# Optimization experiments

Measured on AMD Instinct MI355X. Metric: run time of the kernel, lower is better.

Reference implementation:

```python
import jax, jax.numpy as jnp
import numpy as np

MAX_ROUNDS = 6
MIN_ROUNDS = 2
WINDOW = 4
LAMBDA_P = 0.2
LN_EPS = 1e-5


def _mlp(x, W1, b1, W2, b2):
    # Linear -> exact GELU -> Linear (matches nn.Sequential(Linear, GELU, Linear))
    return jax.nn.gelu(x @ W1 + b1, approximate=False) @ W2 + b2


def _layernorm(x, g, b):
    m = x.mean(-1, keepdims=True)
    v = x.var(-1, keepdims=True)
    return (x - m) / jnp.sqrt(v + LN_EPS) * g + b


def setup_inputs() -> dict:
    key = jax.random.key(0)
    ks = jax.random.split(key, 13)
    B, N, D = 4, 2048, 512
    s = 0.02
    f32 = jnp.float32
    return {
        "summaries": jax.random.normal(ks[0], (B, N, D), f32),
        "msg_W1": jax.random.normal(ks[1], (2 * D, D), f32) * s,
        "msg_b1": jnp.zeros((D,), f32),
        "msg_W2": jax.random.normal(ks[2], (D, D), f32) * s,
        "msg_b2": jnp.zeros((D,), f32),
        "upd_W1": jax.random.normal(ks[3], (2 * D, D), f32) * s,
        "upd_b1": jnp.zeros((D,), f32),
        "upd_W2": jax.random.normal(ks[4], (D, D), f32) * s,
        "upd_b2": jnp.zeros((D,), f32),
        "halt_W": jax.random.normal(ks[5], (D, 1), f32) * s,
        "halt_b": jnp.zeros((1,), f32),
        "ln_g": jnp.ones((D,), f32),
        "ln_b": jnp.zeros((D,), f32),
    }


def reference(summaries, msg_W1, msg_b1, msg_W2, msg_b2,
              upd_W1, upd_b1, upd_W2, upd_b2,
              halt_W, halt_b, ln_g, ln_b):
    B, N, D = summaries.shape
    dt = summaries.dtype
    h = summaries
    remaining = jnp.ones((B, N, 1), dt)
    output = jnp.zeros_like(h)
    kl = jnp.zeros((), dt)
    done = jnp.asarray(False)  # emulates the early `break` under jit
    pos = jnp.arange(N)
    # number of valid causal neighbors of position i: min(i+1, window+1)
    counts = jnp.minimum(pos + 1, WINDOW + 1).astype(dt)[None, :, None]

    for step in range(MAX_ROUNDS):
        # windowed gather + message MLP, vectorized over the (W+1) offsets
        acc = jnp.zeros_like(h)
        for d in range(WINDOW + 1):
            nb = h if d == 0 else jnp.pad(h, ((0, 0), (d, 0), (0, 0)))[:, :N]
            m = _mlp(jnp.concatenate([h, nb], axis=-1), msg_W1, msg_b1, msg_W2, msg_b2)
            mask = (pos >= d).astype(dt)[None, :, None]
            acc = acc + m * mask
        msgs = acc / counts  # mean over valid neighbors, shape (B, N, D)

        new_h = h + _mlp(jnp.concatenate([h, msgs], axis=-1), upd_W1, upd_b1, upd_W2, upd_b2)
        h_next = _layernorm(new_h, ln_g, ln_b)

        if step < MIN_ROUNDS:
            halt = jnp.zeros((B, N, 1), dt)
        elif step == MAX_ROUNDS - 1:
            halt = jnp.ones((B, N, 1), dt)
        else:
            hp = jax.nn.sigmoid(h_next.mean(axis=1, keepdims=True) @ halt_W + halt_b)  # (B,1,1)
            halt = jnp.broadcast_to(hp, (B, N, 1))

        step_weight = remaining * halt
        out_next = output + step_weight * h_next
        rem_next = remaining * (1.0 - halt)

        p_geom = LAMBDA_P * (1.0 - LAMBDA_P) ** step
        # F.kl_div(log(q), log(p), log_target=True) = p * (log p - log q)
        kl_term = p_geom * (jnp.log(p_geom) - jnp.log(halt.mean() + 1e-8))

        active = jnp.logical_not(done)
        af = active.astype(dt)
        h = jnp.where(active, h_next, h)
        output = jnp.where(active, out_next, output)
        remaining = jnp.where(active, rem_next, remaining)
        kl = kl + af * kl_term.astype(dt)
        done = jnp.logical_or(done, remaining.max() < 0.01)

    return output, kl / MAX_ROUNDS
```

## Files before the change

kernel.cpp:

```cpp
#include <hip/hip_runtime.h>
#include <cmath>

#define DEV __device__ __forceinline__

typedef __bf16 bf16x8 __attribute__((ext_vector_type(8)));
typedef float f32x4v __attribute__((ext_vector_type(4)));
typedef unsigned short u16x8 __attribute__((ext_vector_type(8)));
typedef unsigned short u16x4 __attribute__((ext_vector_type(4)));

DEV float bf2f(unsigned short u){ return __uint_as_float(((unsigned)u)<<16); }
DEV unsigned short f2bf(float f){
  unsigned u = __float_as_uint(f);
  u = (u + 0x7fffu + ((u>>16)&1u)) >> 16;
  return (unsigned short)u;
}
DEV float geluf(float x){ return 0.5f*x*(1.0f + erff(x*0.7071067811865475f)); }

#define GLDS16(g,l) __builtin_amdgcn_global_load_lds(\
    (const __attribute__((address_space(1))) void*)(g), \
    (__attribute__((address_space(3))) void*)(l), 16, 0, 0)

#define NB    4
#define NSEQ  2048
#define DDIM  512
#define MROWS 8192

#define OFF_H     0u
#define OFF_HB    16777216u
#define OFF_UV    25165824u
#define OFF_GP    25165824u
#define OFF_R     33554432u
#define OFF_GSC   41943040u
#define OFF_WUV   50331648u
#define OFF_WP    51380224u
#define OFF_WR    52428800u
#define OFF_BUV   52953088u
#define OFF_BP    52957184u
#define OFF_BR    52959232u
#define OFF_DOT   52961280u
#define OFF_SCAL  52994048u
#define OFF_FLAGS 52994112u
#define OFF_A2    25165824u
#define OFF_B2    25690112u

__global__ __launch_bounds__(256) void k_prep_tr(
    const float* __restrict__ mW1, const float* __restrict__ uW2,
    const float* __restrict__ uW1,
    unsigned short* __restrict__ Wuv, unsigned short* __restrict__ Wr,
    unsigned short* __restrict__ Wp,  unsigned short* __restrict__ A2)
{
  __shared__ float t[64][65];
  const int tid = threadIdx.x, c = tid&63, r4 = tid>>6;
  const float* src; unsigned short* dst; int dld;
  switch (blockIdx.y){
    case 0: src = mW1;          dst = Wuv;          dld = 512;  break;
    case 1: src = mW1 + 262144; dst = Wuv + 262144; dld = 512;  break;
    case 2: src = uW2;          dst = Wr;           dld = 512;  break;
    case 3: src = uW1;          dst = Wp;           dld = 1024; break;
    default:src = uW1 + 262144; dst = A2;           dld = 512;  break;
  }
  const int k0 = (blockIdx.x>>3)<<6, n0 = (blockIdx.x&7)<<6;
  #pragma unroll
  for (int i=0;i<16;++i){ int r = i*4 + r4; t[r][c] = src[(size_t)(k0+r)*512 + n0 + c]; }
  __syncthreads();
  #pragma unroll
  for (int i=0;i<16;++i){ int r = i*4 + r4; dst[(size_t)(n0+r)*dld + k0 + c] = f2bf(t[c][r]); }
}

__global__ __launch_bounds__(256) void k_prep_small(
    const float* __restrict__ mW2, const float* __restrict__ mb1,
    const float* __restrict__ ub2,
    unsigned short* __restrict__ B2, float* __restrict__ biasUV,
    float* __restrict__ biasR)
{
  int idx = blockIdx.x*256 + threadIdx.x;
  if (idx < 262144)      B2[idx] = f2bf(mW2[idx]);
  else if (idx < 263168){ int j = idx-262144; biasUV[j] = (j<512)? mb1[j] : 0.f; }
  else if (idx < 263680){ int j = idx-263168; biasR[j] = ub2[j]; }
}

__global__ __launch_bounds__(256) void k_prep_biasP(
    const float* __restrict__ ub1, const float* __restrict__ mb2,
    const float* __restrict__ uW1, float* __restrict__ biasP)
{
  int n = blockIdx.x*256 + threadIdx.x;
  float s = ub1[n];
  for (int j=0;j<512;++j) s += mb2[j]*uW1[(512+j)*512+n];
  biasP[n] = s;
}

__global__ void k_init_state(float* scal, int* flags){
  int t = threadIdx.x;
  if (t<4) scal[t]=1.f;
  else if (t<9) scal[t]=0.f;
  if (t==9){ flags[0]=1; flags[1]=0; }
}

__global__ __launch_bounds__(256) void k_init_h(
    const float* __restrict__ S, float* __restrict__ H, u16x4* __restrict__ Hb)
{
  size_t idx = (size_t)blockIdx.x*256 + threadIdx.x;
  float4 v = ((const float4*)S)[idx];
  ((float4*)H)[idx] = v;
  u16x4 o; o[0]=f2bf(v.x); o[1]=f2bf(v.y); o[2]=f2bf(v.z); o[3]=f2bf(v.w);
  Hb[idx] = o;
}

template<int EPI>
__global__ __launch_bounds__(256) void k_gemm(
    const unsigned short* __restrict__ A0, const unsigned short* __restrict__ A1,
    const unsigned short* __restrict__ Bt, const float* __restrict__ bias,
    void* __restrict__ Cout, int ldc, int ldb, int nK, int ksplit, int gridN,
    const int* __restrict__ flags)
{
  if (flags[0]==0) return;
  __shared__ unsigned short sm[2][12288];
  const int tid = threadIdx.x;
  const int bid = blockIdx.x;
  const int nb  = (int)gridDim.x;
  const int ppx = (nb>>3)/gridN;
  int mp, np;
  if (ppx*gridN*8 == nb){ const int xcd = bid&7, ib = bid>>3; mp = xcd*ppx + ib/gridN; np = ib%gridN; }
  else                  { mp = bid/gridN; np = bid%gridN; }
  const int m0 = mp<<7, n0 = np<<6;
  const int sr = tid>>3;
  const int scA = (((tid&7) ^ (sr&7)) << 3);
  const int lane = tid&63, wv = tid>>6, wr = wv>>1, wc = wv&1;
  const int la = lane&15, lg = lane>>4;
  const int swzr = (la&7)<<3;
  f32x4v acc[4][2] = {};

  auto stage = [&](int ks, int bufi){
    const unsigned short* As = (ks<ksplit)? A0 : A1;
    const int kc = ((ks<ksplit)? ks : (ks-ksplit))<<6;
    unsigned short* s = sm[bufi];
    #pragma unroll
    for (int i=0;i<4;++i)
      GLDS16(As + (size_t)(m0 + i*32 + sr)*512 + kc + scA, s + i*2048 + tid*8);
    #pragma unroll
    for (int i=0;i<2;++i)
      GLDS16(Bt + (size_t)(n0 + i*32 + sr)*ldb + (ks<<6) + scA, s + 8192 + i*2048 + tid*8);
  };

  stage(0, 0);
  if (nK > 1) stage(1, 1);
  for (int ks=0; ks<nK; ++ks){
    const int cur = ks & 1;
    if (ks+1 < nK) asm volatile("s_waitcnt vmcnt(6)" ::: "memory");
    else           asm volatile("s_waitcnt vmcnt(0)" ::: "memory");
    __builtin_amdgcn_s_barrier();
    asm volatile("" ::: "memory");
    const unsigned short* s = sm[cur];
    #pragma unroll
    for (int kk=0;kk<2;++kk){
      bf16x8 af[4], bfr[2];
      #pragma unroll
      for (int mi=0;mi<4;++mi)
        af[mi] = *(const bf16x8*)(s + ((wr<<6) + (mi<<4) + la)*64 + (((kk<<5) + (lg<<3)) ^ swzr));
      #pragma unroll
      for (int ni=0;ni<2;++ni)
        bfr[ni] = *(const bf16x8*)(s + 8192 + ((wc<<5) + (ni<<4) + la)*64 + (((kk<<5) + (lg<<3)) ^ swzr));
      #pragma unroll
      for (int mi=0;mi<4;++mi)
        #pragma unroll
        for (int ni=0;ni<2;++ni)
          acc[mi][ni] = __builtin_amdgcn_mfma_f32_16x16x32_bf16(af[mi], bfr[ni], acc[mi][ni], 0, 0, 0);
    }
    asm volatile("" ::: "memory");
    __builtin_amdgcn_s_barrier();
    asm volatile("" ::: "memory");
    if (ks+2 < nK) stage(ks+2, cur);
  }

  const int r0 = m0 + (wr<<6) + (lg<<2);
  const int c0 = n0 + (wc<<5) + la;
  #pragma unroll
  for (int mi=0;mi<4;++mi){
    #pragma unroll
    for (int ni=0;ni<2;++ni){
      const int col = c0 + (ni<<4);
      const float bs = bias[col];
      #pragma unroll
      for (int r=0;r<4;++r){
        const int row = r0 + (mi<<4) + r;
        float v = acc[mi][ni][r] + bs;
        if constexpr (EPI==1) v = geluf(v);
        if constexpr (EPI==2) ((float*)Cout)[(size_t)row*ldc + col] = v;
        else ((unsigned short*)Cout)[(size_t)row*ldc + col] = f2bf(v);
      }
    }
  }
}

__global__ __launch_bounds__(256) void k_geluacc(
    const unsigned short* __restrict__ UV, unsigned short* __restrict__ G,
    const int* __restrict__ flags)
{
  if (flags[0]==0) return;
  int r = blockIdx.x*4 + (threadIdx.x>>6);
  int lane = threadIdx.x & 63;
  int c8 = lane*8;
  int i = r & (NSEQ-1);
  int nd = (i<4) ? i : 4;
  const u16x8 u = *(const u16x8*)(UV + (size_t)r*1024 + c8);
  float acc[8] = {0,0,0,0,0,0,0,0};
  for (int d=0; d<=nd; ++d){
    const u16x8 v = *(const u16x8*)(UV + (size_t)(r-d)*1024 + 512 + c8);
    #pragma unroll
    for (int j=0;j<8;++j) acc[j] += geluf(bf2f(u[j]) + bf2f(v[j]));
  }
  float inv = 1.0f/(float)(nd+1);
  u16x8 o;
  #pragma unroll
  for (int j=0;j<8;++j) o[j] = f2bf(acc[j]*inv);
  *(u16x8*)(G + (size_t)r*512 + c8) = o;
}

__global__ __launch_bounds__(256) void k_ln(
    const float* __restrict__ Rr, float* __restrict__ H, unsigned short* __restrict__ Hb,
    const float* __restrict__ gamma, const float* __restrict__ beta,
    const float* __restrict__ hW, float* __restrict__ DOT, float* __restrict__ OUT,
    const float* __restrict__ scal, const int* __restrict__ flags,
    int accmode, int dodot)
{
  const int lane = threadIdx.x & 63;
  const int row = (blockIdx.x<<2) + (threadIdx.x>>6);
  const int bidx = row >> 11;
  const size_t base = (size_t)row*512 + lane*8;
  float4 x0 = *(const float4*)(H+base);
  float4 x1 = *(const float4*)(H+base+4);

  if (accmode){
    const float w = scal[4+bidx];
    float4 o0, o1;
    if (accmode==1){
      o0 = make_float4(w*x0.x, w*x0.y, w*x0.z, w*x0.w);
      o1 = make_float4(w*x1.x, w*x1.y, w*x1.z, w*x1.w);
    } else {
      o0 = *(const float4*)(OUT+base);
      o1 = *(const float4*)(OUT+base+4);
      o0.x += w*x0.x; o0.y += w*x0.y; o0.z += w*x0.z; o0.w += w*x0.w;
      o1.x += w*x1.x; o1.y += w*x1.y; o1.z += w*x1.z; o1.w += w*x1.w;
    }
    *(float4*)(OUT+base)   = o0;
    *(float4*)(OUT+base+4) = o1;
  }
  if (flags[0]==0) return;

  float4 r0 = *(const float4*)(Rr+base);
  float4 r1 = *(const float4*)(Rr+base+4);
  x0.x+=r0.x; x0.y+=r0.y; x0.z+=r0.z; x0.w+=r0.w;
  x1.x+=r1.x; x1.y+=r1.y; x1.z+=r1.z; x1.w+=r1.w;
  float s = x0.x+x0.y+x0.z+x0.w + x1.x+x1.y+x1.z+x1.w;
  float q = x0.x*x0.x+x0.y*x0.y+x0.z*x0.z+x0.w*x0.w
          + x1.x*x1.x+x1.y*x1.y+x1.z*x1.z+x1.w*x1.w;
  #pragma unroll
  for (int off=1; off<64; off<<=1){ s += __shfl_xor(s, off); q += __shfl_xor(q, off); }
  const float mean = s*(1.f/512.f);
  const float var  = q*(1.f/512.f) - mean*mean;
  const float rstd = rsqrtf(var + 1e-5f);
  float4 g0 = *(const float4*)(gamma + lane*8);
  float4 g1 = *(const float4*)(gamma + lane*8 + 4);
  float4 b0 = *(const float4*)(beta  + lane*8);
  float4 b1 = *(const float4*)(beta  + lane*8 + 4);
  float y[8];
  y[0]=(x0.x-mean)*rstd*g0.x+b0.x; y[1]=(x0.y-mean)*rstd*g0.y+b0.y;
  y[2]=(x0.z-mean)*rstd*g0.z+b0.z; y[3]=(x0.w-mean)*rstd*g0.w+b0.w;
  y[4]=(x1.x-mean)*rstd*g1.x+b1.x; y[5]=(x1.y-mean)*rstd*g1.y+b1.y;
  y[6]=(x1.z-mean)*rstd*g1.z+b1.z; y[7]=(x1.w-mean)*rstd*g1.w+b1.w;
  *(float4*)(H+base)   = make_float4(y[0],y[1],y[2],y[3]);
  *(float4*)(H+base+4) = make_float4(y[4],y[5],y[6],y[7]);
  u16x8 hb;
  #pragma unroll
  for (int j=0;j<8;++j) hb[j] = f2bf(y[j]);
  *(u16x8*)(Hb+base) = hb;

  if (dodot){
    float4 w0 = *(const float4*)(hW + lane*8);
    float4 w1 = *(const float4*)(hW + lane*8 + 4);
    float d = y[0]*w0.x + y[1]*w0.y + y[2]*w0.z + y[3]*w0.w
            + y[4]*w1.x + y[5]*w1.y + y[6]*w1.z + y[7]*w1.w;
    #pragma unroll
    for (int off=1; off<64; off<<=1) d += __shfl_xor(d, off);
    if (lane==0) DOT[row] = d;
  }
}

__global__ void k_control(const float* __restrict__ DOT, const float* __restrict__ hb,
                          float* __restrict__ scal, int* __restrict__ flags,
                          int step, float p, float logp, float* __restrict__ klout)
{
  __shared__ float hp[4];
  const int t = threadIdx.x, lane = t&63, b = t>>6;
  if (step>=2 && step<5){
    float s = 0.f;
    for (int i=lane; i<NSEQ; i+=64) s += DOT[b*NSEQ + i];
    #pragma unroll
    for (int off=1; off<64; off<<=1) s += __shfl_xor(s, off);
    if (lane==0) hp[b] = s;
  } else if (lane==0) hp[b] = 0.f;
  __syncthreads();
  if (t==0){
    bool active = flags[0]!=0;
    float halt[NB];
    for (int i=0;i<NB;++i){
      if (step < 2) halt[i]=0.f;
      else if (step == 5) halt[i]=1.f;
      else { float z = hp[i]*(1.f/2048.f) + hb[0]; halt[i] = 1.f/(1.f+expf(-z)); }
    }
    float hm = 0.25f*(halt[0]+halt[1]+halt[2]+halt[3]);
    if (active) scal[8] += p*(logp - logf(hm + 1e-8f));
    float mx = 0.f;
    for (int i=0;i<NB;++i){
      float rb = scal[i];
      float w  = active ? rb*halt[i] : 0.f;
      scal[4+i] = w;
      if (active) rb *= (1.f - halt[i]);
      scal[i] = rb;
      mx = fmaxf(mx, rb);
    }
    if (mx < 0.01f) flags[1] = 1;
    flags[0] = flags[1] ? 0 : 1;
    if (step==5) *klout = scal[8]*(1.0f/6.0f);
  }
}

__global__ __launch_bounds__(256) void k_accum(
    const float* __restrict__ H, const float* __restrict__ scal, float* __restrict__ OUT)
{
  size_t idx = (size_t)blockIdx.x*256 + threadIdx.x;
  int b = (int)(idx >> 18);
  float w = scal[4+b];
  float4 h = ((const float4*)H)[idx];
  float4 o = ((float4*)OUT)[idx];
  ((float4*)OUT)[idx] = make_float4(o.x+w*h.x, o.y+w*h.y, o.z+w*h.z, o.w+w*h.w);
}

extern "C" void kernel_launch(void* const* d_in, const int* in_sizes, int n_in,
                              void* d_out, int out_size, void* d_ws, size_t ws_size,
                              hipStream_t stream)
{
  const float* S   = (const float*)d_in[0];
  const float* mW1 = (const float*)d_in[1];
  const float* mb1 = (const float*)d_in[2];
  const float* mW2 = (const float*)d_in[3];
  const float* mb2 = (const float*)d_in[4];
  const float* uW1 = (const float*)d_in[5];
  const float* ub1 = (const float*)d_in[6];
  const float* uW2 = (const float*)d_in[7];
  const float* ub2 = (const float*)d_in[8];
  const float* hW  = (const float*)d_in[9];
  const float* hb  = (const float*)d_in[10];
  const float* lng = (const float*)d_in[11];
  const float* lnb = (const float*)d_in[12];

  char* ws = (char*)d_ws;
  float*          H     = (float*)(ws + OFF_H);
  unsigned short* Hb    = (unsigned short*)(ws + OFF_HB);
  unsigned short* UV    = (unsigned short*)(ws + OFF_UV);
  unsigned short* GP    = (unsigned short*)(ws + OFF_GP);
  unsigned short* GSC   = (unsigned short*)(ws + OFF_GSC);
  float*          Rb    = (float*)(ws + OFF_R);
  unsigned short* Wuv   = (unsigned short*)(ws + OFF_WUV);
  unsigned short* Wp    = (unsigned short*)(ws + OFF_WP);
  unsigned short* Wr    = (unsigned short*)(ws + OFF_WR);
  unsigned short* A2    = (unsigned short*)(ws + OFF_A2);
  unsigned short* B2    = (unsigned short*)(ws + OFF_B2);
  float*          biasUV= (float*)(ws + OFF_BUV);
  float*          biasP = (float*)(ws + OFF_BP);
  float*          biasR = (float*)(ws + OFF_BR);
  float*          DOT   = (float*)(ws + OFF_DOT);
  float*          scal  = (float*)(ws + OFF_SCAL);
  int*            flags = (int*)(ws + OFF_FLAGS);
  float*          OUT   = (float*)d_out;
  float*          klout = OUT + (size_t)NB*NSEQ*DDIM;

  k_init_state<<<1, 256, 0, stream>>>(scal, flags);
  k_prep_tr   <<<dim3(64,5), 256, 0, stream>>>(mW1, uW2, uW1, Wuv, Wr, Wp, A2);
  k_prep_small<<<1032, 256, 0, stream>>>(mW2, mb1, ub2, B2, biasUV, biasR);
  k_prep_biasP<<<2,    256, 0, stream>>>(ub1, mb2, uW1, biasP);
  k_gemm<0><<<32, 256, 0, stream>>>(A2, A2, B2, biasUV+512, Wp+512, 1024, 512, 8, 8, 8, flags);
  k_init_h    <<<4096, 256, 0, stream>>>(S, H, (u16x4*)Hb);

  for (int s = 0; s < 6; ++s){
    k_gemm<0><<<1024, 256, 0, stream>>>(Hb, Hb, Wuv, biasUV, UV, 1024, 512, 8, 8, 16, flags);
    k_geluacc<<<2048, 256, 0, stream>>>(UV, GSC, flags);
    k_gemm<1><<<512, 256, 0, stream>>>(Hb, GSC, Wp, biasP, GP, 512, 1024, 16, 8, 8, flags);
    k_gemm<2><<<512, 256, 0, stream>>>(GP, GP, Wr, biasR, Rb, 512, 512, 8, 8, 8, flags);
    const int accmode = (s==3) ? 1 : (s>=4 ? 2 : 0);
    const int dodot   = (s>=2 && s<=4) ? 1 : 0;
    k_ln<<<2048, 256, 0, stream>>>(Rb, H, Hb, lng, lnb, hW, DOT, OUT, scal, flags, accmode, dodot);
    float p = 0.2f * (float)pow(0.8, (double)s);
    float lp = (float)log((double)p);
    k_control<<<1, 256, 0, stream>>>(DOT, hb, scal, flags, s, p, lp, klout);
  }
  k_accum<<<4096, 256, 0, stream>>>(H, scal, OUT);
}
```

Measured before the change: 580.5 us.

## Fuse U/V message GEMM with windowed GELU accumulation into one kernel

Replaces the separate UV GEMM plus gelu-accumulate kernel with one kernel that computes the U and V projections for a 128x64 tile. It also computes V for the 16 preceding halo rows, stages V in shared memory and does the causal windowed GELU mean in the epilogue. This removes the round trip of the 8192x1024 bf16 UV intermediate through global memory and one kernel launch per round. In exchange it adds redundant halo MFMA work, more LDS usage that can lower occupancy, and a heavier scalar epilogue.

```diff
diff --git a/kernel.cpp b/kernel.cpp
--- a/kernel.cpp
+++ b/kernel.cpp
@@ -27,7 +27,6 @@
 
 #define OFF_H     0u
 #define OFF_HB    16777216u
-#define OFF_UV    25165824u
 #define OFF_GP    25165824u
 #define OFF_R     33554432u
 #define OFF_GSC   41943040u
@@ -192,28 +191,122 @@
   }
 }
 
-__global__ __launch_bounds__(256) void k_geluacc(
-    const unsigned short* __restrict__ UV, unsigned short* __restrict__ G,
+__global__ __launch_bounds__(256) void k_gmsg(
+    const unsigned short* __restrict__ Hb, const unsigned short* __restrict__ Wuv,
+    const float* __restrict__ biasU, unsigned short* __restrict__ G,
     const int* __restrict__ flags)
 {
   if (flags[0]==0) return;
-  int r = blockIdx.x*4 + (threadIdx.x>>6);
-  int lane = threadIdx.x & 63;
-  int c8 = lane*8;
-  int i = r & (NSEQ-1);
-  int nd = (i<4) ? i : 4;
-  const u16x8 u = *(const u16x8*)(UV + (size_t)r*1024 + c8);
-  float acc[8] = {0,0,0,0,0,0,0,0};
-  for (int d=0; d<=nd; ++d){
-    const u16x8 v = *(const u16x8*)(UV + (size_t)(r-d)*1024 + 512 + c8);
-    #pragma unroll
-    for (int j=0;j<8;++j) acc[j] += geluf(bf2f(u[j]) + bf2f(v[j]));
-  }
-  float inv = 1.0f/(float)(nd+1);
-  u16x8 o;
-  #pragma unroll
-  for (int j=0;j<8;++j) o[j] = f2bf(acc[j]*inv);
-  *(u16x8*)(G + (size_t)r*512 + c8) = o;
+  __shared__ __align__(16) unsigned short smraw[2*17408];
+  const int tid = threadIdx.x;
+  const int bid = blockIdx.x;
+  const int xcd = bid & 7, ib = bid >> 3;
+  const int mp = xcd*8 + (ib>>3), np = ib & 7;
+  const int m0 = mp<<7, n0 = np<<6;
+  const int sr = tid>>3;
+  const int scA = (((tid&7) ^ (sr&7)) << 3);
+  const int lane = tid&63, wv = tid>>6, wr = wv>>1, wc = wv&1;
+  const int la = lane&15, lg = lane>>4;
+  const int swzr = (la&7)<<3;
+  f32x4v aU[4][2] = {}, aV[4][2] = {}, aX[2] = {};
+  const int xbase = (m0==0) ? 0 : (m0-16);
+
+  auto stage = [&](int ks, int bufi){
+    const int kc = ks<<6;
+    unsigned short* s = smraw + bufi*17408;
+    #pragma unroll
+    for (int i=0;i<4;++i)
+      GLDS16(Hb + (size_t)(m0 + i*32 + sr)*512 + kc + scA, s + i*2048 + tid*8);
+    if (wv < 2)
+      GLDS16(Hb + (size_t)(xbase + sr)*512 + kc + scA, s + 8192 + tid*8);
+    #pragma unroll
+    for (int i=0;i<2;++i)
+      GLDS16(Wuv + (size_t)(n0 + i*32 + sr)*512 + kc + scA, s + 9216 + i*2048 + tid*8);
+    #pragma unroll
+    for (int i=0;i<2;++i)
+      GLDS16(Wuv + (size_t)(512 + n0 + i*32 + sr)*512 + kc + scA, s + 13312 + i*2048 + tid*8);
+  };
+
+  stage(0, 0);
+  stage(1, 1);
+  for (int ks=0; ks<8; ++ks){
+    const int cur = ks & 1;
+    if (ks+1 < 8){
+      if (wv < 2) asm volatile("s_waitcnt vmcnt(9)" ::: "memory");
+      else        asm volatile("s_waitcnt vmcnt(8)" ::: "memory");
+    } else        asm volatile("s_waitcnt vmcnt(0)" ::: "memory");
+    __builtin_amdgcn_s_barrier();
+    asm volatile("" ::: "memory");
+    const unsigned short* s = smraw + cur*17408;
+    #pragma unroll
+    for (int kk=0;kk<2;++kk){
+      const int ko = ((kk<<5) + (lg<<3)) ^ swzr;
+      bf16x8 af[4], bU[2], bV[2];
+      #pragma unroll
+      for (int mi=0;mi<4;++mi)
+        af[mi] = *(const bf16x8*)(s + ((wr<<6) + (mi<<4) + la)*64 + ko);
+      #pragma unroll
+      for (int ni=0;ni<2;++ni){
+        bU[ni] = *(const bf16x8*)(s + 9216  + (((wc<<5) + (ni<<4) + la))*64 + ko);
+        bV[ni] = *(const bf16x8*)(s + 13312 + (((wc<<5) + (ni<<4) + la))*64 + ko);
+      }
+      #pragma unroll
+      for (int mi=0;mi<4;++mi)
+        #pragma unroll
+        for (int ni=0;ni<2;++ni){
+          aU[mi][ni] = __builtin_amdgcn_mfma_f32_16x16x32_bf16(af[mi], bU[ni], aU[mi][ni], 0, 0, 0);
+          aV[mi][ni] = __builtin_amdgcn_mfma_f32_16x16x32_bf16(af[mi], bV[ni], aV[mi][ni], 0, 0, 0);
+        }
+      if (wr == 0){
+        bf16x8 afx = *(const bf16x8*)(s + 8192 + la*64 + ko);
+        #pragma unroll
+        for (int ni=0;ni<2;++ni)
+          aX[ni] = __builtin_amdgcn_mfma_f32_16x16x32_bf16(afx, bV[ni], aX[ni], 0, 0, 0);
+      }
+    }
+    asm volatile("" ::: "memory");
+    __builtin_amdgcn_s_barrier();
+    asm volatile("" ::: "memory");
+    if (ks+2 < 8) stage(ks+2, cur);
+  }
+
+  float* Vl = (float*)smraw;
+  const int colL = (wc<<5) + la;
+  #pragma unroll
+  for (int mi=0;mi<4;++mi)
+    #pragma unroll
+    for (int ni=0;ni<2;++ni)
+      #pragma unroll
+      for (int q=0;q<4;++q)
+        Vl[(16 + (wr<<6) + (mi<<4) + (lg<<2) + q)*65 + colL + (ni<<4)] = aV[mi][ni][q];
+  if (wr == 0)
+    #pragma unroll
+    for (int ni=0;ni<2;++ni)
+      #pragma unroll
+      for (int q=0;q<4;++q)
+        Vl[((lg<<2) + q)*65 + colL + (ni<<4)] = aX[ni][q];
+  __syncthreads();
+
+  const int ibase = m0 & (NSEQ-1);
+  #pragma unroll
+  for (int mi=0;mi<4;++mi){
+    #pragma unroll
+    for (int ni=0;ni<2;++ni){
+      const int cl = colL + (ni<<4);
+      const float bs = biasU[n0 + cl];
+      #pragma unroll
+      for (int q=0;q<4;++q){
+        const int rl = (wr<<6) + (mi<<4) + (lg<<2) + q;
+        const int i  = ibase + rl;
+        const int nd = (i<4) ? i : 4;
+        const float u = aU[mi][ni][q] + bs;
+        float g = 0.f;
+        for (int d=0; d<=nd; ++d)
+          g += geluf(u + Vl[(16 + rl - d)*65 + cl]);
+        G[(size_t)(m0 + rl)*512 + n0 + cl] = f2bf(g/(float)(nd+1));
+      }
+    }
+  }
 }
 
 __global__ __launch_bounds__(256) void k_ln(
@@ -357,7 +450,6 @@
   char* ws = (char*)d_ws;
   float*          H     = (float*)(ws + OFF_H);
   unsigned short* Hb    = (unsigned short*)(ws + OFF_HB);
-  unsigned short* UV    = (unsigned short*)(ws + OFF_UV);
   unsigned short* GP    = (unsigned short*)(ws + OFF_GP);
   unsigned short* GSC   = (unsigned short*)(ws + OFF_GSC);
   float*          Rb    = (float*)(ws + OFF_R);
@@ -383,8 +475,7 @@
   k_init_h    <<<4096, 256, 0, stream>>>(S, H, (u16x4*)Hb);
 
   for (int s = 0; s < 6; ++s){
-    k_gemm<0><<<1024, 256, 0, stream>>>(Hb, Hb, Wuv, biasUV, UV, 1024, 512, 8, 8, 16, flags);
-    k_geluacc<<<2048, 256, 0, stream>>>(UV, GSC, flags);
+    k_gmsg<<<512, 256, 0, stream>>>(Hb, Wuv, biasUV, GSC, flags);
     k_gemm<1><<<512, 256, 0, stream>>>(Hb, GSC, Wp, biasP, GP, 512, 1024, 16, 8, 8, flags);
     k_gemm<2><<<512, 256, 0, stream>>>(GP, GP, Wr, biasR, Rb, 512, 512, 8, 8, 8, flags);
     const int accmode = (s==3) ? 1 : (s>=4 ? 2 : 0);
```

Measured after the change: 860.3 us. +48.2%, slower.
